# Performance work log

Hardware: AMD Instinct MI355X
Metric: run time of the kernel (lower is better)

## Reference

```python
import jax, jax.numpy as jnp
import numpy as np

N_NODES = 100000
IN_CH = 64
HID = 16
HEADS = 4
OUT_CH = 1
NEG_SLOPE = 0.2
EPS = 1e-16


def gat_conv(x, src, dst, W, att_src, att_dst, bias, heads, out_ch, concat):
    """PyG-style GATConv. src/dst already include self-loops.
    x: [N, F_in]; W: [F_in, heads*out_ch]; att_*: [heads, out_ch]; bias: [heads*out_ch] or [out_ch]."""
    n = x.shape[0]
    h = (x @ W).reshape(n, heads, out_ch)                     # [N,H,C]
    a_src = jnp.einsum('nhc,hc->nh', h, att_src)              # [N,H]
    a_dst = jnp.einsum('nhc,hc->nh', h, att_dst)              # [N,H]
    alpha = jax.nn.leaky_relu(a_src[src] + a_dst[dst], NEG_SLOPE)  # [E,H]
    # segment softmax over incoming edges of each destination node
    m = jax.ops.segment_max(alpha, dst, num_segments=n)       # [N,H]
    e = jnp.exp(alpha - m[dst])
    denom = jax.ops.segment_sum(e, dst, num_segments=n)
    alpha = e / (denom[dst] + EPS)                            # [E,H]
    msg = h[src] * alpha[:, :, None]                          # [E,H,C]
    out = jax.ops.segment_sum(msg, dst, num_segments=n)       # [N,H,C]
    out = out.reshape(n, heads * out_ch) if concat else out.mean(axis=1)
    return out + bias


def setup_inputs() -> dict:
    key = jax.random.key(0)
    ks = jax.random.split(key, 10)
    x = jax.random.normal(ks[0], (N_NODES, IN_CH), dtype=jnp.float32)
    edge_index = jax.random.randint(ks[1], (2, 1600000), 0, N_NODES, dtype=jnp.int64)
    s = 0.1
    W1 = jax.random.normal(ks[2], (IN_CH, HEADS * HID), dtype=jnp.float32) * s
    att_src1 = jax.random.normal(ks[3], (HEADS, HID), dtype=jnp.float32) * s
    att_dst1 = jax.random.normal(ks[4], (HEADS, HID), dtype=jnp.float32) * s
    b1 = jnp.zeros((HEADS * HID,), dtype=jnp.float32)
    W2 = jax.random.normal(ks[5], (HEADS * HID, OUT_CH), dtype=jnp.float32) * s
    att_src2 = jax.random.normal(ks[6], (1, OUT_CH), dtype=jnp.float32) * s
    att_dst2 = jax.random.normal(ks[7], (1, OUT_CH), dtype=jnp.float32) * s
    b2 = jnp.zeros((OUT_CH,), dtype=jnp.float32)
    return {"x": x, "edge_index": edge_index, "W1": W1, "att_src1": att_src1,
            "att_dst1": att_dst1, "b1": b1, "W2": W2, "att_src2": att_src2,
            "att_dst2": att_dst2, "b2": b2}


def reference(x, edge_index, W1, att_src1, att_dst1, b1, W2, att_src2, att_dst2, b2):
    n = x.shape[0]
    loop = jnp.arange(n, dtype=edge_index.dtype)
    src = jnp.concatenate([edge_index[0], loop])  # self-loops (PyG default)
    dst = jnp.concatenate([edge_index[1], loop])
    h = gat_conv(x, src, dst, W1, att_src1, att_dst1, b1, HEADS, HID, concat=True)
    h = jax.nn.elu(h)
    out = gat_conv(h, src, dst, W2, att_src2, att_dst2, b2, 1, OUT_CH, concat=False)
    return out.squeeze()
```

## Files before the change

kernel.cpp:

```cpp
#include <hip/hip_runtime.h>
#include <hip/hip_fp16.h>

#define NN   100000
#define E0   1600000
#define ET   1700000
#define NEG  0.2f
#define EPSV 1e-16f
#define NBK  1563
#define CAP  1536
#define BS   1024
#define NBLK4 ((ET + 4 * BS - 1) / (4 * BS))
#define GEMM_NB 782
#define BC_NB   416
#define E1_NB   6256

typedef _Float16 half8 __attribute__((ext_vector_type(8)));
typedef float f32x16 __attribute__((ext_vector_type(16)));

__global__ __launch_bounds__(256) void k_g1bc(
    const float* __restrict__ x, const int* __restrict__ ei,
    const float* __restrict__ W1, const float* __restrict__ as1,
    const float* __restrict__ ad1,
    __half* __restrict__ h1h, float* __restrict__ asr, float* __restrict__ adr,
    int* __restrict__ bcnt)
{
    int t = threadIdx.x;
    if (blockIdx.x >= GEMM_NB) {
        __shared__ int cnt[NBK];
        for (int i = t; i < NBK; i += 256) cnt[i] = 0;
        __syncthreads();
        int base = (blockIdx.x - GEMM_NB) * (256 * 16);
#pragma unroll
        for (int k = 0; k < 16; ++k) {
            int idx = base + k * 256 + t;
            if (idx < ET) {
                int d = (idx < E0) ? ei[E0 + idx] : (idx - E0);
                atomicAdd(&cnt[d >> 6], 1);
            }
        }
        __syncthreads();
        for (int i = t; i < NBK; i += 256) if (cnt[i]) atomicAdd(&bcnt[i], cnt[i]);
        return;
    }
    __shared__ float Wl[4096];
    __shared__ float Ul[512];
    for (int i = t; i < 4096; i += 256) Wl[i] = W1[i];
    __syncthreads();
    if (t < 64) {
        int k = t;
#pragma unroll
        for (int h = 0; h < 4; ++h) {
            float su = 0.f, du = 0.f;
#pragma unroll
            for (int c = 0; c < 16; ++c) {
                float w = Wl[k * 64 + h * 16 + c];
                su += w * as1[h * 16 + c];
                du += w * ad1[h * 16 + c];
            }
            Ul[k * 8 + h] = su;
            Ul[k * 8 + 4 + h] = du;
        }
    }
    __syncthreads();
    int lane = t & 63, wv = t >> 6;
    int col = lane & 31, q = lane >> 5;
    half8 bf0[4], bf1[4], bf2[4];
#pragma unroll
    for (int kc = 0; kc < 4; ++kc) {
#pragma unroll
        for (int j = 0; j < 8; ++j) {
            int k = kc * 16 + q * 8 + j;
            bf0[kc][j] = (_Float16)Wl[k * 64 + col];
            bf1[kc][j] = (_Float16)Wl[k * 64 + 32 + col];
            bf2[kc][j] = (col < 8) ? (_Float16)Ul[k * 8 + col] : (_Float16)0.f;
        }
    }
    int tile = blockIdx.x * 4 + wv;
    int n0 = tile * 32;
    if (n0 >= NN) return;
    half8 af[4];
    const float* xrow = x + (size_t)(n0 + col) * 64;
#pragma unroll
    for (int kc = 0; kc < 4; ++kc) {
        float4 xa = *(const float4*)(xrow + kc * 16 + q * 8);
        float4 xb = *(const float4*)(xrow + kc * 16 + q * 8 + 4);
        af[kc][0] = (_Float16)xa.x; af[kc][1] = (_Float16)xa.y;
        af[kc][2] = (_Float16)xa.z; af[kc][3] = (_Float16)xa.w;
        af[kc][4] = (_Float16)xb.x; af[kc][5] = (_Float16)xb.y;
        af[kc][6] = (_Float16)xb.z; af[kc][7] = (_Float16)xb.w;
    }
    f32x16 c0 = {}, c1 = {}, c2 = {};
#pragma unroll
    for (int kc = 0; kc < 4; ++kc) {
        c0 = __builtin_amdgcn_mfma_f32_32x32x16_f16(af[kc], bf0[kc], c0, 0, 0, 0);
        c1 = __builtin_amdgcn_mfma_f32_32x32x16_f16(af[kc], bf1[kc], c1, 0, 0, 0);
        c2 = __builtin_amdgcn_mfma_f32_32x32x16_f16(af[kc], bf2[kc], c2, 0, 0, 0);
    }
    int hA = col >> 4, cc = col & 15;
#pragma unroll
    for (int reg = 0; reg < 16; ++reg) {
        int row = (reg & 3) + 8 * (reg >> 2) + 4 * q;
        size_t n = (size_t)(n0 + row);
        h1h[((size_t)hA * NN + n) * 16 + cc]       = __float2half(c0[reg]);
        h1h[((size_t)(hA + 2) * NN + n) * 16 + cc] = __float2half(c1[reg]);
    }
    if (col < 8) {
        float* dst = (col < 4) ? asr : adr;
        int h = col & 3;
#pragma unroll
        for (int reg = 0; reg < 16; ++reg) {
            int row = (reg & 3) + 8 * (reg >> 2) + 4 * q;
            dst[(n0 + row) * 4 + h] = c2[reg];
        }
    }
}

__global__ __launch_bounds__(1024) void k_bscan(const int* __restrict__ bcnt,
                                                int* __restrict__ bbase, int* __restrict__ bcursor)
{
    int t = threadIdx.x;
    int i0 = 2 * t, i1 = 2 * t + 1;
    int a = (i0 < NBK) ? bcnt[i0] : 0;
    int b = (i1 < NBK) ? bcnt[i1] : 0;
    int s = a + b;
    int lane = t & 63, wid = t >> 6;
    int sc = s;
#pragma unroll
    for (int off = 1; off < 64; off <<= 1) {
        int u = __shfl_up(sc, off, 64);
        if (lane >= off) sc += u;
    }
    __shared__ int wsum[16];
    if (lane == 63) wsum[wid] = sc;
    __syncthreads();
    int woff = 0;
    for (int k = 0; k < wid; ++k) woff += wsum[k];
    int excl = sc - s + woff;
    if (i0 < NBK) { bbase[i0] = excl;     bcursor[i0] = excl; }
    if (i1 < NBK) { bbase[i1] = excl + a; bcursor[i1] = excl + a; }
}

__global__ __launch_bounds__(BS) void k_bscat(const int* __restrict__ ei,
                                              int* __restrict__ bcursor, int* __restrict__ bin)
{
    __shared__ int cnt[NBK];
    __shared__ int base[NBK];
    int t = threadIdx.x;
    for (int i = t; i < NBK; i += BS) cnt[i] = 0;
    __syncthreads();
    int blk = blockIdx.x * (BS * 4);
    int b[4], r[4], pk[4];
#pragma unroll
    for (int k = 0; k < 4; ++k) {
        int idx = blk + k * BS + t;
        r[k] = -1;
        if (idx < ET) {
            int s, d;
            if (idx < E0) { s = ei[idx]; d = ei[E0 + idx]; } else { s = d = idx - E0; }
            b[k] = d >> 6;
            pk[k] = s | ((d & 63) << 17);
            r[k] = atomicAdd(&cnt[b[k]], 1);
        }
    }
    __syncthreads();
    for (int i = t; i < NBK; i += BS) if (cnt[i]) base[i] = atomicAdd(&bcursor[i], cnt[i]);
    __syncthreads();
#pragma unroll
    for (int k = 0; k < 4; ++k)
        if (r[k] >= 0) bin[base[b[k]] + r[k]] = pk[k];
}

__global__ __launch_bounds__(256) void k_bsort(
    int* __restrict__ bin, const int* __restrict__ bbase, const int* __restrict__ bcnt,
    const float* __restrict__ asr, const float* __restrict__ adr,
    int* __restrict__ binE01, int* __restrict__ binE23, int* __restrict__ A)
{
    __shared__ int raw[CAP];
    __shared__ int srtS[CAP];
    __shared__ int srtE01[CAP];
    __shared__ int srtE23[CAP];
    __shared__ float adl[256];
    __shared__ int deg[64], cur[64];
    int b = blockIdx.x, t = threadIdx.x;
    int beg = bbase[b], cnt = bcnt[b];
    if (cnt > CAP) cnt = CAP;
    if (t < 64) deg[t] = 0;
    {
        int gi = b * 256 + t;
        adl[t] = (gi < NN * 4) ? adr[gi] : 0.f;
    }
    for (int i = t; i < cnt; i += 256) raw[i] = bin[beg + i];
    __syncthreads();
    for (int i = t; i < cnt; i += 256) atomicAdd(&deg[raw[i] >> 17], 1);
    __syncthreads();
    if (t < 64) {
        int v = deg[t];
        int sc = v;
#pragma unroll
        for (int off = 1; off < 64; off <<= 1) {
            int u = __shfl_up(sc, off, 64);
            if (t >= off) sc += u;
        }
        cur[t] = sc - v;
        int n = b * 64 + t;
        if (n < NN) A[n] = beg + sc;
    }
    __syncthreads();
    for (int i = t; i < cnt; i += 256) {
        int e = raw[i];
        int s = e & 0x1FFFF, dl = e >> 17;
        float4 as4 = *(const float4*)(asr + s * 4);
        int dl4 = dl * 4;
        float a0 = as4.x + adl[dl4 + 0]; a0 = a0 > 0.f ? a0 : NEG * a0;
        float a1 = as4.y + adl[dl4 + 1]; a1 = a1 > 0.f ? a1 : NEG * a1;
        float a2 = as4.z + adl[dl4 + 2]; a2 = a2 > 0.f ? a2 : NEG * a2;
        float a3 = as4.w + adl[dl4 + 3]; a3 = a3 > 0.f ? a3 : NEG * a3;
        __half q0 = __float2half(__expf(a0));
        __half q1 = __float2half(__expf(a1));
        __half q2 = __float2half(__expf(a2));
        __half q3 = __float2half(__expf(a3));
        int r = atomicAdd(&cur[dl], 1);
        srtS[r]   = s;
        srtE01[r] = (int)__half_as_ushort(q0) | ((int)__half_as_ushort(q1) << 16);
        srtE23[r] = (int)__half_as_ushort(q2) | ((int)__half_as_ushort(q3) << 16);
    }
    __syncthreads();
    for (int i = t; i < cnt; i += 256) {
        bin[beg + i]    = srtS[i];
        binE01[beg + i] = srtE01[i];
        binE23[beg + i] = srtE23[i];
    }
}

__global__ __launch_bounds__(256) void k_e1agg(
    const int* __restrict__ binS, const int* __restrict__ binE01,
    const int* __restrict__ binE23, const int* __restrict__ A,
    const int* __restrict__ bbase, const int* __restrict__ bcnt,
    const __half* __restrict__ h1h,
    const float* __restrict__ b1, const float* __restrict__ W2,
    float* __restrict__ g)
{
    __shared__ int lS[CAP];
    __shared__ int lE[CAP];
    int bid = blockIdx.x, t = threadIdx.x;
    int lane8 = bid & 7;
    int h = lane8 >> 1;
    int b = (bid >> 3) * 2 + (lane8 & 1);
    if (b >= NBK) return;
    int beg = bbase[b], cnt = bcnt[b];
    if (cnt > CAP) cnt = CAP;
    const int* binE = (h < 2) ? binE01 : binE23;
    for (int i = t; i < cnt; i += 256) { lS[i] = binS[beg + i]; lE[i] = binE[beg + i]; }
    __syncthreads();
    int q = t & 3, nl = t >> 2;
    int n = b * 64 + nl;
    if (n >= NN) return;
    int je = A[n] - beg;               if (je > cnt) je = cnt;
    int jb = ((n == 0) ? 0 : A[n - 1]) - beg; if (jb < 0) jb = 0;
    size_t hb = (size_t)h * NN;
    int p = q & 1, eo = q >> 1;
    int hsel = h & 1;
    float acc[8];
#pragma unroll
    for (int c = 0; c < 8; ++c) acc[c] = 0.f;
    float den = 0.f;
    for (int base = jb; base < je; base += 2) {
        int e = base + eo;
        if (e < je) {
            int s = lS[e];
            int ew = lE[e];
            unsigned short us = hsel ? (unsigned short)(ew >> 16)
                                     : (unsigned short)(ew & 0xFFFF);
            float evf = __half2float(__ushort_as_half(us));
            den += evf;
            uint4 r0 = *(const uint4*)(h1h + (hb + s) * 16 + p * 8);
            float2 f0 = __half22float2(*(const __half2*)&r0.x);
            float2 f1 = __half22float2(*(const __half2*)&r0.y);
            float2 f2 = __half22float2(*(const __half2*)&r0.z);
            float2 f3 = __half22float2(*(const __half2*)&r0.w);
            acc[0] += evf * f0.x; acc[1] += evf * f0.y;
            acc[2] += evf * f1.x; acc[3] += evf * f1.y;
            acc[4] += evf * f2.x; acc[5] += evf * f2.y;
            acc[6] += evf * f3.x; acc[7] += evf * f3.y;
        }
    }
#pragma unroll
    for (int c = 0; c < 8; ++c) acc[c] += __shfl_xor(acc[c], 2);
    den += __shfl_xor(den, 2);
    float inv = 1.f / (den + EPSV);
    const float* bp = b1 + h * 16 + p * 8;
    const float* wp = W2 + h * 16 + p * 8;
    float gv = 0.f;
#pragma unroll
    for (int c = 0; c < 8; ++c) {
        float v = acc[c] * inv + bp[c];
        v = v > 0.f ? v : __expf(v) - 1.f;
        gv += v * wp[c];
    }
    gv += __shfl_xor(gv, 1);
    if (q == 0) atomicAdd(&g[n], gv);
}

__global__ __launch_bounds__(256) void k_e2agg(
    const int* __restrict__ binS, const int* __restrict__ A,
    const int* __restrict__ bbase, const int* __restrict__ bcnt,
    const float* __restrict__ g, const float* __restrict__ as2,
    const float* __restrict__ ad2, const float* __restrict__ b2,
    float* __restrict__ out)
{
    __shared__ int lcsr[CAP];
    int b = blockIdx.x, t = threadIdx.x;
    int beg = bbase[b], cnt = bcnt[b];
    if (cnt > CAP) cnt = CAP;
    for (int i = t; i < cnt; i += 256) lcsr[i] = binS[beg + i];
    __syncthreads();
    int p = t & 3, nl = t >> 2;
    int n = b * 64 + nl;
    if (n >= NN) return;
    int je = A[n] - beg;               if (je > cnt) je = cnt;
    int jb = ((n == 0) ? 0 : A[n - 1]) - beg; if (jb < 0) jb = 0;
    float cs = as2[0];
    float gdcd = g[n] * ad2[0];
    float acc = 0.f, den = 0.f;
    for (int j = jb + p; j < je; j += 4) {
        float gz = g[lcsr[j]];
        float a = gz * cs + gdcd;
        a = a > 0.f ? a : NEG * a;
        float ev = __expf(a);
        den += ev;
        acc += ev * gz;
    }
    acc += __shfl_xor(acc, 1); den += __shfl_xor(den, 1);
    acc += __shfl_xor(acc, 2); den += __shfl_xor(den, 2);
    if (p == 0) out[n] = acc / (den + EPSV) + b2[0];
}

extern "C" void kernel_launch(void* const* d_in, const int* in_sizes, int n_in,
                              void* d_out, int out_size, void* d_ws, size_t ws_size,
                              hipStream_t stream)
{
    const float* x   = (const float*)d_in[0];
    const int*   ei  = (const int*)d_in[1];
    const float* W1  = (const float*)d_in[2];
    const float* as1 = (const float*)d_in[3];
    const float* ad1 = (const float*)d_in[4];
    const float* b1  = (const float*)d_in[5];
    const float* W2  = (const float*)d_in[6];
    const float* as2 = (const float*)d_in[7];
    const float* ad2 = (const float*)d_in[8];
    const float* b2  = (const float*)d_in[9];
    float* out = (float*)d_out;

    int*   iw      = (int*)d_ws;
    float* fw      = (float*)d_ws;
    int*   bcnt    = iw;
    int*   bbase   = iw + 1664;
    int*   bcursor = iw + 3328;
    int*   A       = iw + 4992;
    int*   bin     = iw + 105344;
    int*   binE01  = iw + 1805344;
    int*   binE23  = iw + 3505344;
    float* asr     = fw + 5205344;
    float* adr     = fw + 5605344;
    float* g       = fw + 6005344;
    __half* h1hQ   = (__half*)(fw + 6105376);

    hipMemsetAsync(bcnt, 0, NBK * sizeof(int), stream);
    hipMemsetAsync(g, 0, NN * sizeof(float), stream);

    k_g1bc  <<<GEMM_NB + BC_NB, 256, 0, stream>>>(x, ei, W1, as1, ad1,
                                                  h1hQ, asr, adr, bcnt);
    k_bscan <<<1, 1024, 0, stream>>>(bcnt, bbase, bcursor);
    k_bscat <<<NBLK4, BS, 0, stream>>>(ei, bcursor, bin);
    k_bsort <<<NBK, 256, 0, stream>>>(bin, bbase, bcnt, asr, adr,
                                      binE01, binE23, A);
    k_e1agg <<<E1_NB, 256, 0, stream>>>(bin, binE01, binE23, A, bbase, bcnt,
                                        h1hQ, b1, W2, g);
    k_e2agg <<<NBK, 256, 0, stream>>>(bin, A, bbase, bcnt, g, as2, ad2, b2, out);
}
```

Baseline: 215.1 us.

## Pack source index and per-head fp16 exp weight into one word per edge

```diff
diff --git a/kernel.cpp b/kernel.cpp
--- a/kernel.cpp
+++ b/kernel.cpp
@@ -173,12 +173,10 @@
 __global__ __launch_bounds__(256) void k_bsort(
     int* __restrict__ bin, const int* __restrict__ bbase, const int* __restrict__ bcnt,
     const float* __restrict__ asr, const float* __restrict__ adr,
-    int* __restrict__ binE01, int* __restrict__ binE23, int* __restrict__ A)
+    int* __restrict__ binH1, int* __restrict__ binH2, int* __restrict__ binH3,
+    int* __restrict__ A)
 {
     __shared__ int raw[CAP];
-    __shared__ int srtS[CAP];
-    __shared__ int srtE01[CAP];
-    __shared__ int srtE23[CAP];
     __shared__ float adl[256];
     __shared__ int deg[64], cur[64];
     int b = blockIdx.x, t = threadIdx.x;
@@ -215,33 +213,29 @@
         float a1 = as4.y + adl[dl4 + 1]; a1 = a1 > 0.f ? a1 : NEG * a1;
         float a2 = as4.z + adl[dl4 + 2]; a2 = a2 > 0.f ? a2 : NEG * a2;
         float a3 = as4.w + adl[dl4 + 3]; a3 = a3 > 0.f ? a3 : NEG * a3;
-        __half q0 = __float2half(__expf(a0));
-        __half q1 = __float2half(__expf(a1));
-        __half q2 = __float2half(__expf(a2));
-        __half q3 = __float2half(__expf(a3));
+        int q0 = (int)__half_as_ushort(__float2half(__expf(a0)));
+        int q1 = (int)__half_as_ushort(__float2half(__expf(a1)));
+        int q2 = (int)__half_as_ushort(__float2half(__expf(a2)));
+        int q3 = (int)__half_as_ushort(__float2half(__expf(a3)));
         int r = atomicAdd(&cur[dl], 1);
-        srtS[r]   = s;
-        srtE01[r] = (int)__half_as_ushort(q0) | ((int)__half_as_ushort(q1) << 16);
-        srtE23[r] = (int)__half_as_ushort(q2) | ((int)__half_as_ushort(q3) << 16);
-    }
-    __syncthreads();
-    for (int i = t; i < cnt; i += 256) {
-        bin[beg + i]    = srtS[i];
-        binE01[beg + i] = srtE01[i];
-        binE23[beg + i] = srtE23[i];
+        int gp = beg + r;
+        bin[gp]   = s | (q0 << 17);
+        binH1[gp] = s | (q1 << 17);
+        binH2[gp] = s | (q2 << 17);
+        binH3[gp] = s | (q3 << 17);
     }
 }
 
 __global__ __launch_bounds__(256) void k_e1agg(
-    const int* __restrict__ binS, const int* __restrict__ binE01,
-    const int* __restrict__ binE23, const int* __restrict__ A,
+    const int* __restrict__ binH0, const int* __restrict__ binH1,
+    const int* __restrict__ binH2, const int* __restrict__ binH3,
+    const int* __restrict__ A,
     const int* __restrict__ bbase, const int* __restrict__ bcnt,
     const __half* __restrict__ h1h,
     const float* __restrict__ b1, const float* __restrict__ W2,
     float* __restrict__ g)
 {
-    __shared__ int lS[CAP];
-    __shared__ int lE[CAP];
+    __shared__ int lw[CAP];
     int bid = blockIdx.x, t = threadIdx.x;
     int lane8 = bid & 7;
     int h = lane8 >> 1;
@@ -249,8 +243,8 @@
     if (b >= NBK) return;
     int beg = bbase[b], cnt = bcnt[b];
     if (cnt > CAP) cnt = CAP;
-    const int* binE = (h < 2) ? binE01 : binE23;
-    for (int i = t; i < cnt; i += 256) { lS[i] = binS[beg + i]; lE[i] = binE[beg + i]; }
+    const int* bh = (h == 0) ? binH0 : (h == 1) ? binH1 : (h == 2) ? binH2 : binH3;
+    for (int i = t; i < cnt; i += 256) lw[i] = bh[beg + i];
     __syncthreads();
     int q = t & 3, nl = t >> 2;
     int n = b * 64 + nl;
@@ -259,30 +253,24 @@
     int jb = ((n == 0) ? 0 : A[n - 1]) - beg; if (jb < 0) jb = 0;
     size_t hb = (size_t)h * NN;
     int p = q & 1, eo = q >> 1;
-    int hsel = h & 1;
     float acc[8];
 #pragma unroll
     for (int c = 0; c < 8; ++c) acc[c] = 0.f;
     float den = 0.f;
-    for (int base = jb; base < je; base += 2) {
-        int e = base + eo;
-        if (e < je) {
-            int s = lS[e];
-            int ew = lE[e];
-            unsigned short us = hsel ? (unsigned short)(ew >> 16)
-                                     : (unsigned short)(ew & 0xFFFF);
-            float evf = __half2float(__ushort_as_half(us));
-            den += evf;
-            uint4 r0 = *(const uint4*)(h1h + (hb + s) * 16 + p * 8);
-            float2 f0 = __half22float2(*(const __half2*)&r0.x);
-            float2 f1 = __half22float2(*(const __half2*)&r0.y);
-            float2 f2 = __half22float2(*(const __half2*)&r0.z);
-            float2 f3 = __half22float2(*(const __half2*)&r0.w);
-            acc[0] += evf * f0.x; acc[1] += evf * f0.y;
-            acc[2] += evf * f1.x; acc[3] += evf * f1.y;
-            acc[4] += evf * f2.x; acc[5] += evf * f2.y;
-            acc[6] += evf * f3.x; acc[7] += evf * f3.y;
-        }
+    for (int e = jb + eo; e < je; e += 2) {
+        int w = lw[e];
+        int s = w & 0x1FFFF;
+        float evf = __half2float(__ushort_as_half((unsigned short)((unsigned)w >> 17)));
+        den += evf;
+        uint4 r0 = *(const uint4*)(h1h + (hb + s) * 16 + p * 8);
+        float2 f0 = __half22float2(*(const __half2*)&r0.x);
+        float2 f1 = __half22float2(*(const __half2*)&r0.y);
+        float2 f2 = __half22float2(*(const __half2*)&r0.z);
+        float2 f3 = __half22float2(*(const __half2*)&r0.w);
+        acc[0] += evf * f0.x; acc[1] += evf * f0.y;
+        acc[2] += evf * f1.x; acc[3] += evf * f1.y;
+        acc[4] += evf * f2.x; acc[5] += evf * f2.y;
+        acc[6] += evf * f3.x; acc[7] += evf * f3.y;
     }
 #pragma unroll
     for (int c = 0; c < 8; ++c) acc[c] += __shfl_xor(acc[c], 2);
@@ -302,7 +290,7 @@
 }
 
 __global__ __launch_bounds__(256) void k_e2agg(
-    const int* __restrict__ binS, const int* __restrict__ A,
+    const int* __restrict__ binH0, const int* __restrict__ A,
     const int* __restrict__ bbase, const int* __restrict__ bcnt,
     const float* __restrict__ g, const float* __restrict__ as2,
     const float* __restrict__ ad2, const float* __restrict__ b2,
@@ -312,7 +300,7 @@
     int b = blockIdx.x, t = threadIdx.x;
     int beg = bbase[b], cnt = bcnt[b];
     if (cnt > CAP) cnt = CAP;
-    for (int i = t; i < cnt; i += 256) lcsr[i] = binS[beg + i];
+    for (int i = t; i < cnt; i += 256) lcsr[i] = binH0[beg + i] & 0x1FFFF;
     __syncthreads();
     int p = t & 3, nl = t >> 2;
     int n = b * 64 + nl;
@@ -358,12 +346,13 @@
     int*   bcursor = iw + 3328;
     int*   A       = iw + 4992;
     int*   bin     = iw + 105344;
-    int*   binE01  = iw + 1805344;
-    int*   binE23  = iw + 3505344;
-    float* asr     = fw + 5205344;
-    float* adr     = fw + 5605344;
-    float* g       = fw + 6005344;
-    __half* h1hQ   = (__half*)(fw + 6105376);
+    int*   binH1   = iw + 1805344;
+    int*   binH2   = iw + 3505344;
+    int*   binH3   = iw + 5205344;
+    float* asr     = fw + 6905344;
+    float* adr     = fw + 7305344;
+    float* g       = fw + 7705344;
+    __half* h1hQ   = (__half*)(fw + 7805376);
 
     hipMemsetAsync(bcnt, 0, NBK * sizeof(int), stream);
     hipMemsetAsync(g, 0, NN * sizeof(float), stream);
@@ -373,8 +362,8 @@
     k_bscan <<<1, 1024, 0, stream>>>(bcnt, bbase, bcursor);
     k_bscat <<<NBLK4, BS, 0, stream>>>(ei, bcursor, bin);
     k_bsort <<<NBK, 256, 0, stream>>>(bin, bbase, bcnt, asr, adr,
-                                      binE01, binE23, A);
-    k_e1agg <<<E1_NB, 256, 0, stream>>>(bin, binE01, binE23, A, bbase, bcnt,
+                                      binH1, binH2, binH3, A);
+    k_e1agg <<<E1_NB, 256, 0, stream>>>(bin, binH1, binH2, binH3, A, bbase, bcnt,
                                         h1hQ, b1, W2, g);
     k_e2agg <<<NBK, 256, 0, stream>>>(bin, A, bbase, bcnt, g, as2, ad2, b2, out);
 }
```

Measured after the change: 224.6 us. +4.4%, slower.
